# Kernel optimization log

Hardware: AMD Instinct MI355X
Metric: run time of the kernel (lower is better)

The kernel has to match this reference:

```python
import jax, jax.numpy as jnp
import numpy as np
from jax import lax

Tx, Ty, NA, NS = 30, 10, 32, 64
HV, MV = 128, 64
B = 16384


def setup_inputs() -> dict:
    key = jax.random.key(0)
    ks = jax.random.split(key, 16)
    g = lambda k, s: jax.random.normal(k, s, jnp.float32) * 0.05
    return {
        "X": jax.random.normal(ks[0], (B, Tx, HV), jnp.float32),
        # pre-attention bidirectional LSTM (PyTorch gate order i,f,g,o; b = b_ih + b_hh)
        "W_ih_f": g(ks[1], (4 * NA, HV)), "W_hh_f": g(ks[2], (4 * NA, NA)), "b_f": g(ks[3], (4 * NA,)),
        "W_ih_r": g(ks[4], (4 * NA, HV)), "W_hh_r": g(ks[5], (4 * NA, NA)), "b_r": g(ks[6], (4 * NA,)),
        # attention MLP
        "W1": g(ks[7], (10, 2 * NA + NS)), "b1": g(ks[8], (10,)),
        "W2": g(ks[9], (1, 10)), "b2": g(ks[10], (1,)),
        # post-attention LSTM cell
        "W_ih_p": g(ks[11], (4 * NS, 2 * NA)), "W_hh_p": g(ks[12], (4 * NS, NS)), "b_p": g(ks[13], (4 * NS,)),
        # output projection
        "Wo": g(ks[14], (MV, NS)), "bo": g(ks[15], (MV,)),
    }


def _cell(x, h, c, W_ih, W_hh, b):
    # PyTorch LSTM cell, gate order (i, f, g, o)
    z = x @ W_ih.T + h @ W_hh.T + b
    i, f, gg, o = jnp.split(z, 4, axis=-1)
    c = jax.nn.sigmoid(f) * c + jax.nn.sigmoid(i) * jnp.tanh(gg)
    h = jax.nn.sigmoid(o) * jnp.tanh(c)
    return h, c


def _run_lstm(X, W_ih, W_hh, b):
    Bn = X.shape[0]
    H = W_hh.shape[1]
    init = (jnp.zeros((Bn, H), X.dtype), jnp.zeros((Bn, H), X.dtype))

    def step(carry, x_t):
        h, c = _cell(x_t, carry[0], carry[1], W_ih, W_hh, b)
        return (h, c), h

    _, hs = lax.scan(step, init, jnp.swapaxes(X, 0, 1))  # hs: [Tx, B, H]
    return jnp.swapaxes(hs, 0, 1)


def reference(X, W_ih_f, W_hh_f, b_f, W_ih_r, W_hh_r, b_r, W1, b1, W2, b2,
              W_ih_p, W_hh_p, b_p, Wo, bo):
    # bidirectional encoder: a is [B, Tx, 2*NA]
    a_f = _run_lstm(X, W_ih_f, W_hh_f, b_f)
    a_r = _run_lstm(X[:, ::-1, :], W_ih_r, W_hh_r, b_r)[:, ::-1, :]
    a = jnp.concatenate([a_f, a_r], axis=-1)
    Bn = X.shape[0]

    def dec_step(carry, _):
        s, c = carry
        # one_step_attention
        s_rep = jnp.broadcast_to(s[:, None, :], (Bn, Tx, NS))
        cat = jnp.concatenate([a, s_rep], axis=-1)          # [B, Tx, 2*NA+NS]
        e = jnp.tanh(cat @ W1.T + b1)                        # [B, Tx, 10]
        en = jax.nn.relu(e @ W2.T + b2)                      # [B, Tx, 1]
        alphas = jax.nn.softmax(en, axis=1)                  # softmax over Tx
        context = jnp.sum(alphas * a, axis=1)                # [B, 2*NA]
        # post-attention LSTM (single step)
        s, c = _cell(context, s, c, W_ih_p, W_hh_p, b_p)
        out = s @ Wo.T + bo                                  # [B, MV]
        return (s, c), out

    init = (jnp.zeros((Bn, NS), X.dtype), jnp.zeros((Bn, NS), X.dtype))
    _, outs = lax.scan(dec_step, init, None, length=Ty)      # [Ty, B, MV]
    return jnp.swapaxes(outs, 0, 1)                          # [B, Ty, MV]
```

## Files before the change

kernel.cpp:

```cpp
#include <hip/hip_runtime.h>

typedef unsigned short u16;
typedef unsigned int   u32;
typedef __attribute__((ext_vector_type(8))) short short8;
typedef __attribute__((ext_vector_type(4))) float f4;

#define BT 8
#define TX 30
#define TY 10

__device__ __forceinline__ float bf2f_u16(u16 h){ u32 i=((u32)h)<<16; float f; __builtin_memcpy(&f,&i,4); return f; }
__device__ __forceinline__ float lo2f(u32 p){ u32 i=p<<16; float f; __builtin_memcpy(&f,&i,4); return f; }
__device__ __forceinline__ float hi2f(u32 p){ u32 i=p&0xffff0000u; float f; __builtin_memcpy(&f,&i,4); return f; }
__device__ __forceinline__ u16 f2bf(float f){ u32 x; __builtin_memcpy(&x,&f,4); u32 r=(x+0x7fffu+((x>>16)&1u))>>16; return (u16)r; }

#if __has_builtin(__builtin_amdgcn_rcpf)
__device__ __forceinline__ float frcp(float x){ return __builtin_amdgcn_rcpf(x); }
#else
__device__ __forceinline__ float frcp(float x){ return 1.0f/x; }
#endif
__device__ __forceinline__ float sigm(float x){ return frcp(1.0f+__expf(-x)); }
__device__ __forceinline__ float tanh_(float x){ x=fminf(fmaxf(x,-15.0f),15.0f); float e=__expf(2.0f*x); return 1.0f - 2.0f*frcp(e+1.0f); }

__device__ __forceinline__ f4 mfma16(short8 a, short8 b, f4 c){
    return __builtin_amdgcn_mfma_f32_16x16x32_bf16(a, b, c, 0, 0, 0);
}

union S8u { short8 s; u32 u[4]; };

__device__ __forceinline__ void cvt_pair(float a0, float a1, u32& hp, u32& lp){
    u32 u0, u1; __builtin_memcpy(&u0,&a0,4); __builtin_memcpy(&u1,&a1,4);
    hp = __builtin_amdgcn_perm(u1, u0, 0x07060302u);
    float r0 = a0 - hi2f(u0);
    float r1 = a1 - hi2f(u1);
    u32 v0, v1; __builtin_memcpy(&v0,&r0,4); __builtin_memcpy(&v1,&r1,4);
    lp = __builtin_amdgcn_perm(v1, v0, 0x07060302u);
}

struct SDec {
    float w1[10][132];
    float aW1[BT][TX][10];
    u16 sh[16][72], sl[16][72];
    u16 ctxh[16][72], ctxl[16][72];
    float sW1[BT][12];
    float en[BT][32];
    float w2b[12]; float b2s;
};
struct SEnc {
    u16 h[2][2][2][BT][40];
    u16 zr[40];
};
union UU { SEnc e; SDec d; };
struct Smem {
    u16 a[BT][TX][72];
    UU u;
};

__global__ __launch_bounds__(256, 2) void fused_kernel(
    const float* __restrict__ X,
    const float* __restrict__ Wihf, const float* __restrict__ Whhf, const float* __restrict__ bfv,
    const float* __restrict__ Wihr, const float* __restrict__ Whhr, const float* __restrict__ brv,
    const float* __restrict__ W1, const float* __restrict__ b1, const float* __restrict__ W2, const float* __restrict__ b2,
    const float* __restrict__ Wihp, const float* __restrict__ Whhp, const float* __restrict__ bp,
    const float* __restrict__ Wo, const float* __restrict__ bo,
    float* __restrict__ out)
{
    __shared__ __align__(16) Smem sm;
    const int tid = threadIdx.x;
    const int b0  = blockIdx.x * BT;

    {
        u32* p = (u32*)&sm;
        for (int i = tid; i < (int)(sizeof(Smem)/4); i += 256) p[i] = 0u;
    }
    __syncthreads();

    const int lane = tid & 63;
    const int wv   = tid >> 6;
    const int mL   = lane & 15;
    const int qL   = lane >> 4;
    const int k0q  = qL * 8;
    const int ed   = wv >> 1;
    const int ub   = (wv & 1) * 16;
    const int sstep= mL >> 3;

    const float* Wih = ed ? Wihr : Wihf;
    const float* Whh = ed ? Whhr : Whhf;
    const float* bv  = ed ? brv  : bfv;

    short8 Bih[4][4]; short8 Bhh[4]; float bias4[4];
    #pragma unroll
    for (int gt = 0; gt < 4; gt++){
        const int n = gt*32 + ub + mL;
        #pragma unroll
        for (int kt = 0; kt < 4; kt++){
            const float* p = Wih + n*128 + kt*32 + k0q;
            short8 s;
            #pragma unroll
            for (int j = 0; j < 8; j++) s[j] = (short)f2bf(p[j]);
            Bih[gt][kt] = s;
        }
        {
            const float* p = Whh + n*32 + k0q;
            short8 s;
            #pragma unroll
            for (int j = 0; j < 8; j++) s[j] = (short)f2bf(p[j]);
            Bhh[gt] = s;
        }
        bias4[gt] = bv[n];
    }

    const float* xrow = X + ((long)(b0 + (mL & 7))) * TX * 128;
    float cst[4] = {0.f,0.f,0.f,0.f};

    auto epair = [&](int t, f4* cur, f4* nxt){
        if (t + 2 < TX){
            const int ts = ed ? (TX-1-(t+2+sstep)) : (t+2+sstep);
            const float* p = xrow + ts*128 + k0q;
            #pragma unroll
            for (int kt = 0; kt < 4; kt++){
                nxt[2*kt]   = *(const f4*)(p + kt*32);
                nxt[2*kt+1] = *(const f4*)(p + kt*32 + 4);
            }
        }
        const int rb = (t+1) & 1, wb = t & 1;

        f4 acc[4];
        #pragma unroll
        for (int gt = 0; gt < 4; gt++) acc[gt] = (f4){bias4[gt],bias4[gt],bias4[gt],bias4[gt]};

        #pragma unroll
        for (int kt = 0; kt < 4; kt++){
            S8u xh, xl;
            #pragma unroll
            for (int pp = 0; pp < 4; pp++){
                const f4 v = cur[2*kt + (pp>>1)];
                const int e = (pp & 1) * 2;
                cvt_pair(v[e], v[e+1], xh.u[pp], xl.u[pp]);
            }
            #pragma unroll
            for (int gt = 0; gt < 4; gt++){
                acc[gt] = mfma16(xh.s, Bih[gt][kt], acc[gt]);
                acc[gt] = mfma16(xl.s, Bih[gt][kt], acc[gt]);
            }
        }
        {
            const short8 Ahh = *(const short8*)((mL < 8) ? &sm.u.e.h[rb][ed][0][mL][k0q] : &sm.u.e.zr[k0q]);
            const short8 Ahl = *(const short8*)((mL < 8) ? &sm.u.e.h[rb][ed][1][mL][k0q] : &sm.u.e.zr[k0q]);
            #pragma unroll
            for (int gt = 0; gt < 4; gt++){
                acc[gt] = mfma16(Ahh, Bhh[gt], acc[gt]);
                acc[gt] = mfma16(Ahl, Bhh[gt], acc[gt]);
            }
        }
        if (qL < 2){
            const int tpos = ed ? (TX-1-t) : t;
            #pragma unroll
            for (int reg = 0; reg < 4; reg++){
                const int m = qL*4 + reg;
                const float ii = sigm(acc[0][reg]), ff = sigm(acc[1][reg]);
                const float gg = tanh_(acc[2][reg]), oo = sigm(acc[3][reg]);
                cst[reg] = ff*cst[reg] + ii*gg;
                const float hh = oo * tanh_(cst[reg]);
                const u16 hhi = f2bf(hh);
                const u16 hlo = f2bf(hh - bf2f_u16(hhi));
                sm.u.e.h[wb][ed][0][m][ub+mL] = hhi;
                sm.u.e.h[wb][ed][1][m][ub+mL] = hlo;
                sm.a[m][tpos][ed*32 + ub + mL] = hhi;
            }
        }
        #pragma unroll
        for (int reg = 0; reg < 4; reg++) cst[reg] = __shfl_xor(cst[reg], 32);
        __syncthreads();
        {
            const short8 Ahh = *(const short8*)((mL >= 8) ? &sm.u.e.h[wb][ed][0][mL-8][k0q] : &sm.u.e.zr[k0q]);
            const short8 Ahl = *(const short8*)((mL >= 8) ? &sm.u.e.h[wb][ed][1][mL-8][k0q] : &sm.u.e.zr[k0q]);
            #pragma unroll
            for (int gt = 0; gt < 4; gt++){
                acc[gt] = mfma16(Ahh, Bhh[gt], acc[gt]);
                acc[gt] = mfma16(Ahl, Bhh[gt], acc[gt]);
            }
        }
        if (qL >= 2){
            const int tpos = ed ? (TX-2-t) : (t+1);
            #pragma unroll
            for (int reg = 0; reg < 4; reg++){
                const int m = (qL-2)*4 + reg;
                const float ii = sigm(acc[0][reg]), ff = sigm(acc[1][reg]);
                const float gg = tanh_(acc[2][reg]), oo = sigm(acc[3][reg]);
                cst[reg] = ff*cst[reg] + ii*gg;
                const float hh = oo * tanh_(cst[reg]);
                const u16 hhi = f2bf(hh);
                const u16 hlo = f2bf(hh - bf2f_u16(hhi));
                sm.u.e.h[rb][ed][0][m][ub+mL] = hhi;
                sm.u.e.h[rb][ed][1][m][ub+mL] = hlo;
                sm.a[m][tpos][ed*32 + ub + mL] = hhi;
            }
        }
        #pragma unroll
        for (int reg = 0; reg < 4; reg++) cst[reg] = __shfl_xor(cst[reg], 32);
        __syncthreads();
    };

    f4 rawA[8], rawB[8];
    {
        const int ts0 = ed ? (TX-1-sstep) : sstep;
        const float* p = xrow + ts0*128 + k0q;
        #pragma unroll
        for (int kt = 0; kt < 4; kt++){
            rawA[2*kt]   = *(const f4*)(p + kt*32);
            rawA[2*kt+1] = *(const f4*)(p + kt*32 + 4);
        }
    }
    for (int tp = 0; tp < 28; tp += 4){ epair(tp, rawA, rawB); epair(tp+2, rawB, rawA); }
    epair(28, rawA, rawB);

    for (int i = tid; i < 1280; i += 256){ const int j = i >> 7, k = i & 127; sm.u.d.w1[j][k] = W1[i]; }
    { u32* z = (u32*)sm.u.d.sh; for (int i = tid; i < 4*16*72/2; i += 256) z[i] = 0u; }
    if (tid < 10) sm.u.d.w2b[tid] = W2[tid];
    if (tid == 0) sm.u.d.b2s = b2[0];
    __syncthreads();

    if (tid < 240){
        const int er = tid/30, et = tid - er*30;
        float accj[10];
        #pragma unroll
        for (int j = 0; j < 10; j++) accj[j] = b1[j];
        const u32* arow = (const u32*)&sm.a[er][et][0];
        for (int k2 = 0; k2 < 32; k2++){
            const u32 pa = arow[k2];
            const float a0 = lo2f(pa), a1 = hi2f(pa);
            #pragma unroll
            for (int j = 0; j < 10; j++)
                accj[j] += a0*sm.u.d.w1[j][2*k2] + a1*sm.u.d.w1[j][2*k2+1];
        }
        #pragma unroll
        for (int j = 0; j < 10; j++) sm.u.d.aW1[er][et][j] = accj[j];
    }

    const int uw = wv * 16;
    short8 Bip[4][2], Bhp[4][2]; float pb4[4];
    #pragma unroll
    for (int gt = 0; gt < 4; gt++){
        const int n = gt*64 + uw + mL;
        #pragma unroll
        for (int kt = 0; kt < 2; kt++){
            const float* p = Wihp + n*64 + kt*32 + k0q;
            const float* q = Whhp + n*64 + kt*32 + k0q;
            short8 s1v, s2v;
            #pragma unroll
            for (int j = 0; j < 8; j++){ s1v[j] = (short)f2bf(p[j]); s2v[j] = (short)f2bf(q[j]); }
            Bip[gt][kt] = s1v; Bhp[gt][kt] = s2v;
        }
        pb4[gt] = bp[n];
    }
    short8 Bo2[2];
    {
        const int n = uw + mL;
        #pragma unroll
        for (int kt = 0; kt < 2; kt++){
            const float* p = Wo + n*64 + kt*32 + k0q;
            short8 s;
            #pragma unroll
            for (int j = 0; j < 8; j++) s[j] = (short)f2bf(p[j]);
            Bo2[kt] = s;
        }
    }
    short8 W1sB[2];
    #pragma unroll
    for (int kt = 0; kt < 2; kt++){
        short8 s;
        #pragma unroll
        for (int j = 0; j < 8; j++){
            const float v = (mL < 10) ? W1[mL*128 + 64 + kt*32 + k0q + j] : 0.f;
            s[j] = (short)f2bf(v);
        }
        W1sB[kt] = s;
    }
    const float boL = bo[uw + mL];
    float cs2[4] = {0.f,0.f,0.f,0.f};
    __syncthreads();

    for (int ty = 0; ty < TY; ty++){
        {
            f4 accW = (f4){0.f,0.f,0.f,0.f};
            #pragma unroll
            for (int kt = 0; kt < 2; kt++){
                const short8 shh = *(const short8*)&sm.u.d.sh[mL][kt*32 + k0q];
                const short8 sll = *(const short8*)&sm.u.d.sl[mL][kt*32 + k0q];
                accW = mfma16(shh, W1sB[kt], accW);
                accW = mfma16(sll, W1sB[kt], accW);
            }
            if (qL < 2 && mL < 10 && wv == 0){
                #pragma unroll
                for (int reg = 0; reg < 4; reg++) sm.u.d.sW1[qL*4+reg][mL] = accW[reg];
            }
        }
        __syncthreads();
        if (tid < 240){
            const int er = tid/30, et = tid - er*30;
            float env = sm.u.d.b2s;
            #pragma unroll
            for (int j = 0; j < 10; j++){
                const float z = sm.u.d.aW1[er][et][j] + sm.u.d.sW1[er][j];
                env += sm.u.d.w2b[j]*tanh_(z);
            }
            sm.u.d.en[er][et] = fmaxf(env, 0.f);
        }
        __syncthreads();
        {
            const int cr = tid >> 5, cup = tid & 31;
            const float* enr = sm.u.d.en[cr];
            float mx = enr[0];
            #pragma unroll
            for (int t2 = 1; t2 < TX; t2++) mx = fmaxf(mx, enr[t2]);
            float ssum = 0.f, s0 = 0.f, s1 = 0.f;
            const u16* ap = &sm.a[cr][0][2*cup];
            #pragma unroll 5
            for (int t2 = 0; t2 < TX; t2++){
                const float e = __expf(enr[t2]-mx);
                const u32 pa = *(const u32*)(ap + t2*72);
                ssum += e;
                s0 += e*lo2f(pa); s1 += e*hi2f(pa);
            }
            const float inv = frcp(ssum);
            s0 *= inv; s1 *= inv;
            const u16 h0 = f2bf(s0), h1 = f2bf(s1);
            const u16 l0 = f2bf(s0 - bf2f_u16(h0)), l1 = f2bf(s1 - bf2f_u16(h1));
            *(u32*)&sm.u.d.ctxh[cr][2*cup] = (u32)h0 | ((u32)h1 << 16);
            *(u32*)&sm.u.d.ctxl[cr][2*cup] = (u32)l0 | ((u32)l1 << 16);
        }
        __syncthreads();
        f4 acc2[4];
        #pragma unroll
        for (int gt = 0; gt < 4; gt++) acc2[gt] = (f4){pb4[gt],pb4[gt],pb4[gt],pb4[gt]};
        #pragma unroll
        for (int kt = 0; kt < 2; kt++){
            const short8 ch  = *(const short8*)&sm.u.d.ctxh[mL][kt*32 + k0q];
            const short8 cl  = *(const short8*)&sm.u.d.ctxl[mL][kt*32 + k0q];
            const short8 shh = *(const short8*)&sm.u.d.sh[mL][kt*32 + k0q];
            const short8 sll = *(const short8*)&sm.u.d.sl[mL][kt*32 + k0q];
            #pragma unroll
            for (int gt = 0; gt < 4; gt++){
                acc2[gt] = mfma16(ch,  Bip[gt][kt], acc2[gt]);
                acc2[gt] = mfma16(cl,  Bip[gt][kt], acc2[gt]);
                acc2[gt] = mfma16(shh, Bhp[gt][kt], acc2[gt]);
                acc2[gt] = mfma16(sll, Bhp[gt][kt], acc2[gt]);
            }
        }
        __syncthreads();
        if (qL < 2){
            #pragma unroll
            for (int reg = 0; reg < 4; reg++){
                const int m = qL*4 + reg;
                const float ii = sigm(acc2[0][reg]), ff = sigm(acc2[1][reg]);
                const float gg = tanh_(acc2[2][reg]), oo = sigm(acc2[3][reg]);
                cs2[reg] = ff*cs2[reg] + ii*gg;
                const float sv = oo * tanh_(cs2[reg]);
                const u16 shi = f2bf(sv);
                const u16 slo = f2bf(sv - bf2f_u16(shi));
                sm.u.d.sh[m][uw+mL]  = shi;
                sm.u.d.sl[m][uw+mL]  = slo;
            }
        }
        __syncthreads();
        f4 acc3 = (f4){boL, boL, boL, boL};
        #pragma unroll
        for (int kt = 0; kt < 2; kt++){
            const short8 shh = *(const short8*)&sm.u.d.sh[mL][kt*32 + k0q];
            const short8 sll = *(const short8*)&sm.u.d.sl[mL][kt*32 + k0q];
            acc3 = mfma16(shh, Bo2[kt], acc3);
            acc3 = mfma16(sll, Bo2[kt], acc3);
        }
        if (qL < 2){
            #pragma unroll
            for (int reg = 0; reg < 4; reg++){
                const int m = qL*4 + reg;
                out[(((long)(b0+m))*TY + ty)*64 + uw + mL] = acc3[reg];
            }
        }
    }
}

extern "C" void kernel_launch(void* const* d_in, const int* in_sizes, int n_in,
                              void* d_out, int out_size, void* d_ws, size_t ws_size,
                              hipStream_t stream) {
    const float* X    = (const float*)d_in[0];
    const float* Wihf = (const float*)d_in[1];
    const float* Whhf = (const float*)d_in[2];
    const float* bfv  = (const float*)d_in[3];
    const float* Wihr = (const float*)d_in[4];
    const float* Whhr = (const float*)d_in[5];
    const float* brv  = (const float*)d_in[6];
    const float* W1   = (const float*)d_in[7];
    const float* b1   = (const float*)d_in[8];
    const float* W2   = (const float*)d_in[9];
    const float* b2   = (const float*)d_in[10];
    const float* Wihp = (const float*)d_in[11];
    const float* Whhp = (const float*)d_in[12];
    const float* bp   = (const float*)d_in[13];
    const float* Wo   = (const float*)d_in[14];
    const float* bo   = (const float*)d_in[15];
    float* out = (float*)d_out;

    const int B = in_sizes[0] / (TX * 128);
    dim3 grid(B / BT), block(256);
    hipLaunchKernelGGL(fused_kernel, grid, block, 0, stream,
                       X, Wihf, Whhf, bfv, Wihr, Whhr, brv,
                       W1, b1, W2, b2, Wihp, Whhp, bp, Wo, bo, out);
}
```

Measured before the change: 651.0 us.

## Compute attention aW1 with MFMA and shrink decoder LDS for three blocks per CU

Replaces the scalar per-thread a·W1 precomputation, which staged W1 in shared memory, with bf16 MFMA tiles using a hi/lo split of W1 held in registers. The decoder state and context buffers drop from 16 to 8 rows, and the unused rows read from a shared zero row instead. The full-Smem zero fill is narrowed to the encoder region only. Together these cut LDS use so launch bounds can request three blocks per CU, at the risk of register spilling under the tighter register budget.

```diff
diff --git a/kernel.cpp b/kernel.cpp
--- a/kernel.cpp
+++ b/kernel.cpp
@@ -38,10 +38,10 @@
 }
 
 struct SDec {
-    float w1[10][132];
     float aW1[BT][TX][10];
-    u16 sh[16][72], sl[16][72];
-    u16 ctxh[16][72], ctxl[16][72];
+    u16 sh[BT][72], sl[BT][72];
+    u16 ctxh[BT][72], ctxl[BT][72];
+    u16 zr2[72];
     float sW1[BT][12];
     float en[BT][32];
     float w2b[12]; float b2s;
@@ -56,7 +56,7 @@
     UU u;
 };
 
-__global__ __launch_bounds__(256, 2) void fused_kernel(
+__global__ __launch_bounds__(256, 3) void fused_kernel(
     const float* __restrict__ X,
     const float* __restrict__ Wihf, const float* __restrict__ Whhf, const float* __restrict__ bfv,
     const float* __restrict__ Wihr, const float* __restrict__ Whhr, const float* __restrict__ brv,
@@ -70,8 +70,8 @@
     const int b0  = blockIdx.x * BT;
 
     {
-        u32* p = (u32*)&sm;
-        for (int i = tid; i < (int)(sizeof(Smem)/4); i += 256) p[i] = 0u;
+        u32* p = (u32*)&sm.u.e;
+        for (int i = tid; i < (int)(sizeof(SEnc)/4); i += 256) p[i] = 0u;
     }
     __syncthreads();
 
@@ -215,27 +215,44 @@
     for (int tp = 0; tp < 28; tp += 4){ epair(tp, rawA, rawB); epair(tp+2, rawB, rawA); }
     epair(28, rawA, rawB);
 
-    for (int i = tid; i < 1280; i += 256){ const int j = i >> 7, k = i & 127; sm.u.d.w1[j][k] = W1[i]; }
-    { u32* z = (u32*)sm.u.d.sh; for (int i = tid; i < 4*16*72/2; i += 256) z[i] = 0u; }
+    {
+        u32* z = (u32*)sm.u.d.sh;
+        for (int i = tid; i < (4*BT*72 + 72)/2; i += 256) z[i] = 0u;
+    }
     if (tid < 10) sm.u.d.w2b[tid] = W2[tid];
     if (tid == 0) sm.u.d.b2s = b2[0];
-    __syncthreads();
-
-    if (tid < 240){
-        const int er = tid/30, et = tid - er*30;
-        float accj[10];
-        #pragma unroll
-        for (int j = 0; j < 10; j++) accj[j] = b1[j];
-        const u32* arow = (const u32*)&sm.a[er][et][0];
-        for (int k2 = 0; k2 < 32; k2++){
-            const u32 pa = arow[k2];
-            const float a0 = lo2f(pa), a1 = hi2f(pa);
-            #pragma unroll
-            for (int j = 0; j < 10; j++)
-                accj[j] += a0*sm.u.d.w1[j][2*k2] + a1*sm.u.d.w1[j][2*k2+1];
-        }
-        #pragma unroll
-        for (int j = 0; j < 10; j++) sm.u.d.aW1[er][et][j] = accj[j];
+
+    short8 W1aB[2][2];
+    #pragma unroll
+    for (int kt = 0; kt < 2; kt++){
+        short8 hv8, lv8;
+        #pragma unroll
+        for (int j = 0; j < 8; j++){
+            const float v = (mL < 10) ? W1[mL*128 + kt*32 + k0q + j] : 0.f;
+            const u16 hb = f2bf(v);
+            hv8[j] = (short)hb;
+            lv8[j] = (short)f2bf(v - bf2f_u16(hb));
+        }
+        W1aB[kt][0] = hv8; W1aB[kt][1] = lv8;
+    }
+    const float b1v = (mL < 10) ? b1[mL] : 0.f;
+
+    for (int tile = wv; tile < 15; tile += 4){
+        f4 accA = (f4){b1v, b1v, b1v, b1v};
+        const u16* abase = &sm.a[0][0][0] + (tile*16 + mL)*72;
+        #pragma unroll
+        for (int kt = 0; kt < 2; kt++){
+            const short8 av = *(const short8*)(abase + kt*32 + k0q);
+            accA = mfma16(av, W1aB[kt][0], accA);
+            accA = mfma16(av, W1aB[kt][1], accA);
+        }
+        if (mL < 10){
+            #pragma unroll
+            for (int reg = 0; reg < 4; reg++){
+                const int r = tile*16 + qL*4 + reg;
+                (&sm.u.d.aW1[0][0][0])[r*10 + mL] = accA[reg];
+            }
+        }
     }
 
     const int uw = wv * 16;
@@ -286,8 +303,9 @@
             f4 accW = (f4){0.f,0.f,0.f,0.f};
             #pragma unroll
             for (int kt = 0; kt < 2; kt++){
-                const short8 shh = *(const short8*)&sm.u.d.sh[mL][kt*32 + k0q];
-                const short8 sll = *(const short8*)&sm.u.d.sl[mL][kt*32 + k0q];
+                const int ko = kt*32 + k0q;
+                const short8 shh = *(const short8*)((mL < 8) ? &sm.u.d.sh[mL][ko] : &sm.u.d.zr2[ko]);
+                const short8 sll = *(const short8*)((mL < 8) ? &sm.u.d.sl[mL][ko] : &sm.u.d.zr2[ko]);
                 accW = mfma16(shh, W1sB[kt], accW);
                 accW = mfma16(sll, W1sB[kt], accW);
             }
@@ -336,10 +354,12 @@
         for (int gt = 0; gt < 4; gt++) acc2[gt] = (f4){pb4[gt],pb4[gt],pb4[gt],pb4[gt]};
         #pragma unroll
         for (int kt = 0; kt < 2; kt++){
-            const short8 ch  = *(const short8*)&sm.u.d.ctxh[mL][kt*32 + k0q];
-            const short8 cl  = *(const short8*)&sm.u.d.ctxl[mL][kt*32 + k0q];
-            const short8 shh = *(const short8*)&sm.u.d.sh[mL][kt*32 + k0q];
-            const short8 sll = *(const short8*)&sm.u.d.sl[mL][kt*32 + k0q];
+            const int ko = kt*32 + k0q;
+            const bool v8 = (mL < 8);
+            const short8 ch  = *(const short8*)(v8 ? &sm.u.d.ctxh[mL][ko] : &sm.u.d.zr2[ko]);
+            const short8 cl  = *(const short8*)(v8 ? &sm.u.d.ctxl[mL][ko] : &sm.u.d.zr2[ko]);
+            const short8 shh = *(const short8*)(v8 ? &sm.u.d.sh[mL][ko]   : &sm.u.d.zr2[ko]);
+            const short8 sll = *(const short8*)(v8 ? &sm.u.d.sl[mL][ko]   : &sm.u.d.zr2[ko]);
             #pragma unroll
             for (int gt = 0; gt < 4; gt++){
                 acc2[gt] = mfma16(ch,  Bip[gt][kt], acc2[gt]);
@@ -367,8 +387,9 @@
         f4 acc3 = (f4){boL, boL, boL, boL};
         #pragma unroll
         for (int kt = 0; kt < 2; kt++){
-            const short8 shh = *(const short8*)&sm.u.d.sh[mL][kt*32 + k0q];
-            const short8 sll = *(const short8*)&sm.u.d.sl[mL][kt*32 + k0q];
+            const int ko = kt*32 + k0q;
+            const short8 shh = *(const short8*)((mL < 8) ? &sm.u.d.sh[mL][ko] : &sm.u.d.zr2[ko]);
+            const short8 sll = *(const short8*)((mL < 8) ? &sm.u.d.sl[mL][ko] : &sm.u.d.zr2[ko]);
             acc3 = mfma16(shh, Bo2[kt], acc3);
             acc3 = mfma16(sll, Bo2[kt], acc3);
         }
```

Result: slower. 752.9 us (+15.6%).
